# Kernel tuning notes

Measured on AMD Instinct MI355X. Metric: run time of the kernel, lower is better.

Reference implementation:

```python
import jax, jax.numpy as jnp
import numpy as np

# Dimensions
B, S = 4, 1024            # sequences, tokens per sequence (prefill: q_len == kv_len)
NQO, NKV, D = 32, 8, 128  # GQA heads
BS = 16                   # page (block) size
NUM_BLOCKS = 512
BLOCKS_PER_SEQ = S // BS  # 64
SCALE = 1.0 / float(np.sqrt(D))


def setup_inputs() -> dict:
    key = jax.random.key(0)
    k1, k2, k3 = jax.random.split(key, 3)
    query = jax.random.normal(k1, (B * S, NQO * D), dtype=jnp.float32)
    key_t = jax.random.normal(k2, (B * S, NKV * D), dtype=jnp.float32)
    value = jax.random.normal(k3, (B * S, NKV * D), dtype=jnp.float32)

    # Paged layout: each sequence owns BLOCKS_PER_SEQ distinct blocks (shuffled).
    rng = np.random.default_rng(0)
    perm = rng.permutation(NUM_BLOCKS)[: B * BLOCKS_PER_SEQ]
    block_tables = perm.reshape(B, BLOCKS_PER_SEQ).astype(np.int32)
    tok = np.arange(S)
    # flat slot index for token t of sequence b: block_id * BS + offset
    slots = block_tables[:, tok // BS] * BS + (tok % BS)  # [B, S]
    new_cache_slots = jnp.asarray(slots.reshape(-1), dtype=jnp.int32)

    key_cache = jnp.zeros((NUM_BLOCKS, BS, NKV, D), dtype=jnp.float32)
    value_cache = jnp.zeros((NUM_BLOCKS, BS, NKV, D), dtype=jnp.float32)
    return {
        "query": query,
        "key": key_t,
        "value": value,
        "key_cache": key_cache,
        "value_cache": value_cache,
        "new_cache_slots": new_cache_slots,
        "block_tables": jnp.asarray(block_tables),
    }


def reference(query, key, value, key_cache, value_cache, new_cache_slots, block_tables):
    q = query.reshape(B * S, NQO, D)
    k = key.reshape(B * S, NKV, D)
    v = value.reshape(B * S, NKV, D)

    # Scatter new K/V into paged cache (kv_cache.set_kv_cache)
    kc = key_cache.reshape(NUM_BLOCKS * BS, NKV, D).at[new_cache_slots].set(k)
    vc = value_cache.reshape(NUM_BLOCKS * BS, NKV, D).at[new_cache_slots].set(v)

    # Gather per-sequence contiguous KV via block tables
    slot = (block_tables[:, :, None] * BS + jnp.arange(BS)).reshape(B, S)  # [B,S]
    kseq = kc[slot]  # [B, S, NKV, D]
    vseq = vc[slot]  # [B, S, NKV, D]

    G = NQO // NKV
    qb = q.reshape(B, S, NKV, G, D)
    scores = jnp.einsum("bqhgd,bkhd->bhgqk", qb, kseq) * SCALE

    # causal mask (q_len == kv_len here; general rule: k_pos <= kv_len - q_len + q_pos)
    qpos = jnp.arange(S)[:, None]
    kpos = jnp.arange(S)[None, :]
    scores = jnp.where(qpos >= kpos, scores, -jnp.inf)

    probs = jax.nn.softmax(scores, axis=-1)
    out = jnp.einsum("bhgqk,bkhd->bqhgd", probs, vseq)
    return out.reshape(B * S, NQO * D)
```

## Files before the change

### kernel.cpp

```cpp
#include <hip/hip_runtime.h>

typedef __attribute__((ext_vector_type(8))) short bf16x8;
typedef __attribute__((ext_vector_type(16))) float f32x16;
typedef __attribute__((ext_vector_type(4))) unsigned uint4v;
typedef __attribute__((ext_vector_type(2))) unsigned uint2v;

#define MFMA32(a, b, c) __builtin_amdgcn_mfma_f32_32x32x16_bf16((a), (b), (c), 0, 0, 0)

__device__ __forceinline__ unsigned pk2(float lo, float hi) {
  unsigned r;
  asm("v_cvt_pk_bf16_f32 %0, %1, %2" : "=v"(r) : "v"(lo), "v"(hi));
  return r;
}

__device__ __forceinline__ float fexp2(float x) {
  float y; asm("v_exp_f32 %0, %1" : "=v"(y) : "v"(x)); return y;
}

__device__ __forceinline__ f32x16 zero16() {
  f32x16 z;
#pragma unroll
  for (int i = 0; i < 16; ++i) z[i] = 0.0f;
  return z;
}

constexpr int S_ = 1024, D = 128;
constexpr int QSTR = 32 * 128;
constexpr int KSTR = 8 * 128;
constexpr float QSCL = 0.12751741f;

__global__ __launch_bounds__(512, 2) void fa_kernel(
    const float* __restrict__ Qg, const float* __restrict__ Kg,
    const float* __restrict__ Vg, float* __restrict__ Og) {
  const int bid  = blockIdx.x;
  const int hkv  = bid & 7;
  const int b    = (bid >> 3) & 3;
  const int qt64 = 15 - (bid >> 5);
  const int h4   = hkv << 2;

  const int tid  = threadIdx.x;
  const int wid  = tid >> 6;
  const int lane = tid & 63;
  const int r    = lane & 31;
  const int hi   = lane >> 5;

  const int g     = wid & 3;
  const int strip = wid >> 2;
  const int h     = h4 + g;
  const int wq0   = (qt64 << 6) + (strip << 5);
  const int qrow  = wq0 + r;

  __shared__ __align__(16) unsigned char Kl0[64 * 256];
  __shared__ __align__(16) unsigned char Vl0[128 * 128];
  __shared__ __align__(16) unsigned char Kl1[64 * 256];
  __shared__ __align__(16) unsigned char Vl1[128 * 128];

  bf16x8 qf[8];
  {
    const float* qp = Qg + (size_t)(b * S_ + qrow) * QSTR + h * D;
#pragma unroll
    for (int c = 0; c < 8; ++c) {
      const float4* p4 = (const float4*)(qp + 16 * c + 8 * hi);
      float4 x = p4[0], y = p4[1];
      uint4v w = (uint4v){pk2(x.x * QSCL, x.y * QSCL), pk2(x.z * QSCL, x.w * QSCL),
                          pk2(y.x * QSCL, y.y * QSCL), pk2(y.z * QSCL, y.w * QSCL)};
      qf[c] = __builtin_bit_cast(bf16x8, w);
    }
  }

  const int kvrow = tid >> 3;
  const int dbase = (tid & 7) << 4;
  const float* kbase = Kg + (size_t)(b * S_) * KSTR + hkv * D;
  const int vd   = tid & 127;
  const int vkvb = (tid >> 7) << 4;
  const float* vbase = Vg + (size_t)(b * S_) * KSTR + hkv * D;

  float4 kreg[4];
  float  vreg[16];

  auto ISSUE = [&](int kv0) {
    const float4* kp = (const float4*)(kbase + (size_t)(kv0 + kvrow) * KSTR + dbase);
#pragma unroll
    for (int j = 0; j < 4; ++j) kreg[j] = kp[j];
    const float* vp = vbase + (size_t)(kv0 + vkvb) * KSTR + vd;
#pragma unroll
    for (int kk = 0; kk < 16; ++kk) vreg[kk] = vp[kk * KSTR];
  };

  auto WRITE = [&](unsigned char* Kl, unsigned char* Vl) {
#pragma unroll
    for (int ss = 0; ss < 2; ++ss) {
      float4 x = kreg[2 * ss], y = kreg[2 * ss + 1];
      uint4v w = (uint4v){pk2(x.x, x.y), pk2(x.z, x.w), pk2(y.x, y.y), pk2(y.z, y.w)};
      const int slot = (dbase >> 3) + ss;
      *(uint4v*)(Kl + kvrow * 256 + ((slot ^ (kvrow & 7)) << 4)) = w;
    }
#pragma unroll
    for (int ss = 0; ss < 2; ++ss) {
      uint4v w = (uint4v){pk2(vreg[8 * ss + 0], vreg[8 * ss + 1]),
                          pk2(vreg[8 * ss + 2], vreg[8 * ss + 3]),
                          pk2(vreg[8 * ss + 4], vreg[8 * ss + 5]),
                          pk2(vreg[8 * ss + 6], vreg[8 * ss + 7])};
      const int slot = (vkvb >> 3) + ss;
      *(uint4v*)(Vl + vd * 128 + ((slot ^ (vd & 7)) << 4)) = w;
    }
  };

  f32x16 o0 = zero16(), o1 = zero16(), o2 = zero16(), o3 = zero16();
  float m = -1e30f, lsum = 0.0f;

  auto COMPUTE = [&](const unsigned char* Kl, const unsigned char* Vl, int kv0) {
    f32x16 s0 = zero16(), s1 = zero16();
    __builtin_amdgcn_s_setprio(1);
#pragma unroll
    for (int c = 0; c < 8; ++c) {
      const int so = (((2 * c + hi) ^ (r & 7)) << 4);
      bf16x8 k0 = *(const bf16x8*)(Kl + r * 256 + so);
      bf16x8 k1 = *(const bf16x8*)(Kl + (32 + r) * 256 + so);
      s0 = MFMA32(k0, qf[c], s0);
      s1 = MFMA32(k1, qf[c], s1);
    }
    __builtin_amdgcn_s_setprio(0);

    if (kv0 + 63 > wq0) {
#pragma unroll
      for (int rr = 0; rr < 16; ++rr) {
        const int R = (rr & 3) + ((rr >> 2) << 3) + (hi << 2);
        if (kv0 + R > qrow)      s0[rr] = -1e30f;
        if (kv0 + 32 + R > qrow) s1[rr] = -1e30f;
      }
    }

    float mt = fmaxf(s0[0], s1[0]);
#pragma unroll
    for (int rr = 1; rr < 16; ++rr) mt = fmaxf(mt, fmaxf(s0[rr], s1[rr]));
    mt = fmaxf(mt, __shfl_xor(mt, 32));

    if (__any(mt > m + 6.0f)) {
      const float mn = fmaxf(m, mt);
      const float sc = fexp2(m - mn);
      m = mn;
      lsum *= sc;
#pragma unroll
      for (int rr = 0; rr < 16; ++rr) {
        const float srow = __shfl(sc, (rr & 3) + ((rr >> 2) << 3) + (hi << 2));
        o0[rr] *= srow; o1[rr] *= srow; o2[rr] *= srow; o3[rr] *= srow;
      }
    }

    float ps = 0.0f;
    bf16x8 A0, A1, A2, A3;
    {
      float p[16];
#pragma unroll
      for (int rr = 0; rr < 16; ++rr) { p[rr] = fexp2(s0[rr] - m); ps += p[rr]; }
      unsigned d0 = pk2(p[0], p[1]),   d1 = pk2(p[2], p[3]);
      unsigned d2 = pk2(p[4], p[5]),   d3 = pk2(p[6], p[7]);
      unsigned d4 = pk2(p[8], p[9]),   d5 = pk2(p[10], p[11]);
      unsigned d6 = pk2(p[12], p[13]), d7 = pk2(p[14], p[15]);
      uint2v w02 = __builtin_amdgcn_permlane32_swap(d0, d2, false, false);
      uint2v w13 = __builtin_amdgcn_permlane32_swap(d1, d3, false, false);
      uint2v w46 = __builtin_amdgcn_permlane32_swap(d4, d6, false, false);
      uint2v w57 = __builtin_amdgcn_permlane32_swap(d5, d7, false, false);
      A0 = __builtin_bit_cast(bf16x8, (uint4v){w02[0], w13[0], w02[1], w13[1]});
      A1 = __builtin_bit_cast(bf16x8, (uint4v){w46[0], w57[0], w46[1], w57[1]});
    }
    {
      float p[16];
#pragma unroll
      for (int rr = 0; rr < 16; ++rr) { p[rr] = fexp2(s1[rr] - m); ps += p[rr]; }
      unsigned d0 = pk2(p[0], p[1]),   d1 = pk2(p[2], p[3]);
      unsigned d2 = pk2(p[4], p[5]),   d3 = pk2(p[6], p[7]);
      unsigned d4 = pk2(p[8], p[9]),   d5 = pk2(p[10], p[11]);
      unsigned d6 = pk2(p[12], p[13]), d7 = pk2(p[14], p[15]);
      uint2v w02 = __builtin_amdgcn_permlane32_swap(d0, d2, false, false);
      uint2v w13 = __builtin_amdgcn_permlane32_swap(d1, d3, false, false);
      uint2v w46 = __builtin_amdgcn_permlane32_swap(d4, d6, false, false);
      uint2v w57 = __builtin_amdgcn_permlane32_swap(d5, d7, false, false);
      A2 = __builtin_bit_cast(bf16x8, (uint4v){w02[0], w13[0], w02[1], w13[1]});
      A3 = __builtin_bit_cast(bf16x8, (uint4v){w46[0], w57[0], w46[1], w57[1]});
    }
    lsum += ps;

    __builtin_amdgcn_s_setprio(1);
#pragma unroll
    for (int t = 0; t < 4; ++t) {
      const bf16x8 pf = (t == 0) ? A0 : (t == 1) ? A1 : (t == 2) ? A2 : A3;
      const int so = (((2 * t + hi) ^ (r & 7)) << 4);
      bf16x8 v0 = *(const bf16x8*)(Vl + r * 128 + so);
      bf16x8 v1 = *(const bf16x8*)(Vl + (32 + r) * 128 + so);
      bf16x8 v2 = *(const bf16x8*)(Vl + (64 + r) * 128 + so);
      bf16x8 v3 = *(const bf16x8*)(Vl + (96 + r) * 128 + so);
      o0 = MFMA32(pf, v0, o0);
      o1 = MFMA32(pf, v1, o1);
      o2 = MFMA32(pf, v2, o2);
      o3 = MFMA32(pf, v3, o3);
    }
    __builtin_amdgcn_s_setprio(0);
  };

  const int nt = qt64 + 1;

  ISSUE(0);
  WRITE(Kl0, Vl0);
  if (nt > 1) ISSUE(64);

  unsigned char *Kc = Kl0, *Vc = Vl0, *Kn = Kl1, *Vn = Vl1;
  for (int t = 0; t < nt; ++t) {
    __syncthreads();
    COMPUTE(Kc, Vc, t << 6);
    if (t + 1 < nt) {
      WRITE(Kn, Vn);
      if (t + 2 < nt) ISSUE((t + 2) << 6);
      unsigned char* tp;
      tp = Kc; Kc = Kn; Kn = tp;
      tp = Vc; Vc = Vn; Vn = tp;
    }
  }

  float lt = lsum + __shfl_xor(lsum, 32);
#pragma unroll
  for (int rr = 0; rr < 16; ++rr) {
    const int R = (rr & 3) + ((rr >> 2) << 3) + (hi << 2);
    const float li = __shfl(lt, R);
    const float inv = 1.0f / li;
    float* op = Og + (size_t)(b * S_ + wq0 + R) * QSTR + h * D + r;
    op[0]  = o0[rr] * inv;
    op[32] = o1[rr] * inv;
    op[64] = o2[rr] * inv;
    op[96] = o3[rr] * inv;
  }
}

extern "C" void kernel_launch(void* const* d_in, const int* in_sizes, int n_in,
                              void* d_out, int out_size, void* d_ws, size_t ws_size,
                              hipStream_t stream) {
  const float* Q = (const float*)d_in[0];
  const float* K = (const float*)d_in[1];
  const float* V = (const float*)d_in[2];
  float* O = (float*)d_out;
  fa_kernel<<<dim3(512), dim3(512), 0, stream>>>(Q, K, V, O);
}
```

Baseline: 63.59 us.

## Switch to 16x16x32 MFMA with 16 waves per block and staggered load/compute

Replaces the 32x32x16 MFMA tiling with 16x16x32 MFMAs, so each wave handles 16 query rows and the block grows to 1024 threads (16 waves), halving per-thread K/V staging and accumulator registers. The P-to-A-operand relayout now uses shuffles instead of permlane32 swaps. Alternate strips order the global-to-LDS write before or after compute to spread memory and MFMA activity. This raises occupancy and parallelism but adds shuffle overhead, and each K/V LDS tile is now read by twice as many waves.

```diff
diff --git a/kernel.cpp b/kernel.cpp
--- a/kernel.cpp
+++ b/kernel.cpp
@@ -1,11 +1,10 @@
 #include <hip/hip_runtime.h>
 
 typedef __attribute__((ext_vector_type(8))) short bf16x8;
-typedef __attribute__((ext_vector_type(16))) float f32x16;
+typedef __attribute__((ext_vector_type(4))) float f32x4;
 typedef __attribute__((ext_vector_type(4))) unsigned uint4v;
-typedef __attribute__((ext_vector_type(2))) unsigned uint2v;
-
-#define MFMA32(a, b, c) __builtin_amdgcn_mfma_f32_32x32x16_bf16((a), (b), (c), 0, 0, 0)
+
+#define MFMA16(a, b, c) __builtin_amdgcn_mfma_f32_16x16x32_bf16((a), (b), (c), 0, 0, 0)
 
 __device__ __forceinline__ unsigned pk2(float lo, float hi) {
   unsigned r;
@@ -17,11 +16,8 @@
   float y; asm("v_exp_f32 %0, %1" : "=v"(y) : "v"(x)); return y;
 }
 
-__device__ __forceinline__ f32x16 zero16() {
-  f32x16 z;
-#pragma unroll
-  for (int i = 0; i < 16; ++i) z[i] = 0.0f;
-  return z;
+__device__ __forceinline__ f32x4 zero4() {
+  return (f32x4){0.0f, 0.0f, 0.0f, 0.0f};
 }
 
 constexpr int S_ = 1024, D = 128;
@@ -29,38 +25,37 @@
 constexpr int KSTR = 8 * 128;
 constexpr float QSCL = 0.12751741f;
 
-__global__ __launch_bounds__(512, 2) void fa_kernel(
+__global__ __launch_bounds__(1024, 4) void fa_kernel(
     const float* __restrict__ Qg, const float* __restrict__ Kg,
     const float* __restrict__ Vg, float* __restrict__ Og) {
   const int bid  = blockIdx.x;
   const int hkv  = bid & 7;
   const int b    = (bid >> 3) & 3;
   const int qt64 = 15 - (bid >> 5);
-  const int h4   = hkv << 2;
 
   const int tid  = threadIdx.x;
   const int wid  = tid >> 6;
   const int lane = tid & 63;
-  const int r    = lane & 31;
-  const int hi   = lane >> 5;
+  const int q16  = lane & 15;
+  const int lg   = lane >> 4;
 
   const int g     = wid & 3;
   const int strip = wid >> 2;
-  const int h     = h4 + g;
-  const int wq0   = (qt64 << 6) + (strip << 5);
-  const int qrow  = wq0 + r;
+  const int h     = (hkv << 2) + g;
+  const int wq0   = (qt64 << 6) + (strip << 4);
+  const int qrow  = wq0 + q16;
 
   __shared__ __align__(16) unsigned char Kl0[64 * 256];
   __shared__ __align__(16) unsigned char Vl0[128 * 128];
   __shared__ __align__(16) unsigned char Kl1[64 * 256];
   __shared__ __align__(16) unsigned char Vl1[128 * 128];
 
-  bf16x8 qf[8];
+  bf16x8 qf[4];
   {
     const float* qp = Qg + (size_t)(b * S_ + qrow) * QSTR + h * D;
 #pragma unroll
-    for (int c = 0; c < 8; ++c) {
-      const float4* p4 = (const float4*)(qp + 16 * c + 8 * hi);
+    for (int c = 0; c < 4; ++c) {
+      const float4* p4 = (const float4*)(qp + 32 * c + 8 * lg);
       float4 x = p4[0], y = p4[1];
       uint4v w = (uint4v){pk2(x.x * QSCL, x.y * QSCL), pk2(x.z * QSCL, x.w * QSCL),
                           pk2(y.x * QSCL, y.y * QSCL), pk2(y.z * QSCL, y.w * QSCL)};
@@ -68,72 +63,73 @@
     }
   }
 
-  const int kvrow = tid >> 3;
-  const int dbase = (tid & 7) << 4;
+  const int kvrow = tid >> 4;
+  const int dbase = (tid & 15) << 3;
   const float* kbase = Kg + (size_t)(b * S_) * KSTR + hkv * D;
   const int vd   = tid & 127;
-  const int vkvb = (tid >> 7) << 4;
+  const int vkvb = (tid >> 7) << 3;
   const float* vbase = Vg + (size_t)(b * S_) * KSTR + hkv * D;
 
-  float4 kreg[4];
-  float  vreg[16];
+  float4 kreg[2];
+  float  vreg[8];
 
   auto ISSUE = [&](int kv0) {
     const float4* kp = (const float4*)(kbase + (size_t)(kv0 + kvrow) * KSTR + dbase);
-#pragma unroll
-    for (int j = 0; j < 4; ++j) kreg[j] = kp[j];
+    kreg[0] = kp[0];
+    kreg[1] = kp[1];
     const float* vp = vbase + (size_t)(kv0 + vkvb) * KSTR + vd;
 #pragma unroll
-    for (int kk = 0; kk < 16; ++kk) vreg[kk] = vp[kk * KSTR];
+    for (int kk = 0; kk < 8; ++kk) vreg[kk] = vp[kk * KSTR];
   };
 
   auto WRITE = [&](unsigned char* Kl, unsigned char* Vl) {
-#pragma unroll
-    for (int ss = 0; ss < 2; ++ss) {
-      float4 x = kreg[2 * ss], y = kreg[2 * ss + 1];
-      uint4v w = (uint4v){pk2(x.x, x.y), pk2(x.z, x.w), pk2(y.x, y.y), pk2(y.z, y.w)};
-      const int slot = (dbase >> 3) + ss;
-      *(uint4v*)(Kl + kvrow * 256 + ((slot ^ (kvrow & 7)) << 4)) = w;
-    }
-#pragma unroll
-    for (int ss = 0; ss < 2; ++ss) {
-      uint4v w = (uint4v){pk2(vreg[8 * ss + 0], vreg[8 * ss + 1]),
-                          pk2(vreg[8 * ss + 2], vreg[8 * ss + 3]),
-                          pk2(vreg[8 * ss + 4], vreg[8 * ss + 5]),
-                          pk2(vreg[8 * ss + 6], vreg[8 * ss + 7])};
-      const int slot = (vkvb >> 3) + ss;
-      *(uint4v*)(Vl + vd * 128 + ((slot ^ (vd & 7)) << 4)) = w;
-    }
+    uint4v wk = (uint4v){pk2(kreg[0].x, kreg[0].y), pk2(kreg[0].z, kreg[0].w),
+                         pk2(kreg[1].x, kreg[1].y), pk2(kreg[1].z, kreg[1].w)};
+    *(uint4v*)(Kl + kvrow * 256 + (((tid & 15) ^ (kvrow & 7)) << 4)) = wk;
+    uint4v wv = (uint4v){pk2(vreg[0], vreg[1]), pk2(vreg[2], vreg[3]),
+                         pk2(vreg[4], vreg[5]), pk2(vreg[6], vreg[7])};
+    *(uint4v*)(Vl + vd * 128 + (((tid >> 7) ^ (vd & 7)) << 4)) = wv;
   };
 
-  f32x16 o0 = zero16(), o1 = zero16(), o2 = zero16(), o3 = zero16();
+  f32x4 o0 = zero4(), o1 = zero4(), o2 = zero4(), o3 = zero4();
+  f32x4 o4 = zero4(), o5 = zero4(), o6 = zero4(), o7 = zero4();
   float m = -1e30f, lsum = 0.0f;
 
   auto COMPUTE = [&](const unsigned char* Kl, const unsigned char* Vl, int kv0) {
-    f32x16 s0 = zero16(), s1 = zero16();
+    f32x4 s0 = zero4(), s1 = zero4(), s2 = zero4(), s3 = zero4();
     __builtin_amdgcn_s_setprio(1);
 #pragma unroll
-    for (int c = 0; c < 8; ++c) {
-      const int so = (((2 * c + hi) ^ (r & 7)) << 4);
-      bf16x8 k0 = *(const bf16x8*)(Kl + r * 256 + so);
-      bf16x8 k1 = *(const bf16x8*)(Kl + (32 + r) * 256 + so);
-      s0 = MFMA32(k0, qf[c], s0);
-      s1 = MFMA32(k1, qf[c], s1);
+    for (int c = 0; c < 4; ++c) {
+      const int so = ((4 * c + lg) ^ (q16 & 7)) << 4;
+      const unsigned char* Kb = Kl + q16 * 256 + so;
+      bf16x8 k0 = *(const bf16x8*)(Kb);
+      bf16x8 k1 = *(const bf16x8*)(Kb + 16 * 256);
+      bf16x8 k2 = *(const bf16x8*)(Kb + 32 * 256);
+      bf16x8 k3 = *(const bf16x8*)(Kb + 48 * 256);
+      s0 = MFMA16(k0, qf[c], s0);
+      s1 = MFMA16(k1, qf[c], s1);
+      s2 = MFMA16(k2, qf[c], s2);
+      s3 = MFMA16(k3, qf[c], s3);
     }
     __builtin_amdgcn_s_setprio(0);
 
     if (kv0 + 63 > wq0) {
+      const int kvb_ = kv0 + 4 * lg;
 #pragma unroll
-      for (int rr = 0; rr < 16; ++rr) {
-        const int R = (rr & 3) + ((rr >> 2) << 3) + (hi << 2);
-        if (kv0 + R > qrow)      s0[rr] = -1e30f;
-        if (kv0 + 32 + R > qrow) s1[rr] = -1e30f;
+      for (int reg = 0; reg < 4; ++reg) {
+        if (kvb_ + reg > qrow)      s0[reg] = -1e30f;
+        if (kvb_ + 16 + reg > qrow) s1[reg] = -1e30f;
+        if (kvb_ + 32 + reg > qrow) s2[reg] = -1e30f;
+        if (kvb_ + 48 + reg > qrow) s3[reg] = -1e30f;
       }
     }
 
-    float mt = fmaxf(s0[0], s1[0]);
-#pragma unroll
-    for (int rr = 1; rr < 16; ++rr) mt = fmaxf(mt, fmaxf(s0[rr], s1[rr]));
+    float x0 = fmaxf(fmaxf(s0[0], s1[0]), fmaxf(s2[0], s3[0]));
+    float x1 = fmaxf(fmaxf(s0[1], s1[1]), fmaxf(s2[1], s3[1]));
+    float x2 = fmaxf(fmaxf(s0[2], s1[2]), fmaxf(s2[2], s3[2]));
+    float x3 = fmaxf(fmaxf(s0[3], s1[3]), fmaxf(s2[3], s3[3]));
+    float mt = fmaxf(fmaxf(x0, x1), fmaxf(x2, x3));
+    mt = fmaxf(mt, __shfl_xor(mt, 16));
     mt = fmaxf(mt, __shfl_xor(mt, 32));
 
     if (__any(mt > m + 6.0f)) {
@@ -141,60 +137,110 @@
       const float sc = fexp2(m - mn);
       m = mn;
       lsum *= sc;
-#pragma unroll
-      for (int rr = 0; rr < 16; ++rr) {
-        const float srow = __shfl(sc, (rr & 3) + ((rr >> 2) << 3) + (hi << 2));
-        o0[rr] *= srow; o1[rr] *= srow; o2[rr] *= srow; o3[rr] *= srow;
-      }
-    }
-
-    float ps = 0.0f;
-    bf16x8 A0, A1, A2, A3;
-    {
-      float p[16];
-#pragma unroll
-      for (int rr = 0; rr < 16; ++rr) { p[rr] = fexp2(s0[rr] - m); ps += p[rr]; }
-      unsigned d0 = pk2(p[0], p[1]),   d1 = pk2(p[2], p[3]);
-      unsigned d2 = pk2(p[4], p[5]),   d3 = pk2(p[6], p[7]);
-      unsigned d4 = pk2(p[8], p[9]),   d5 = pk2(p[10], p[11]);
-      unsigned d6 = pk2(p[12], p[13]), d7 = pk2(p[14], p[15]);
-      uint2v w02 = __builtin_amdgcn_permlane32_swap(d0, d2, false, false);
-      uint2v w13 = __builtin_amdgcn_permlane32_swap(d1, d3, false, false);
-      uint2v w46 = __builtin_amdgcn_permlane32_swap(d4, d6, false, false);
-      uint2v w57 = __builtin_amdgcn_permlane32_swap(d5, d7, false, false);
-      A0 = __builtin_bit_cast(bf16x8, (uint4v){w02[0], w13[0], w02[1], w13[1]});
-      A1 = __builtin_bit_cast(bf16x8, (uint4v){w46[0], w57[0], w46[1], w57[1]});
-    }
-    {
-      float p[16];
-#pragma unroll
-      for (int rr = 0; rr < 16; ++rr) { p[rr] = fexp2(s1[rr] - m); ps += p[rr]; }
-      unsigned d0 = pk2(p[0], p[1]),   d1 = pk2(p[2], p[3]);
-      unsigned d2 = pk2(p[4], p[5]),   d3 = pk2(p[6], p[7]);
-      unsigned d4 = pk2(p[8], p[9]),   d5 = pk2(p[10], p[11]);
-      unsigned d6 = pk2(p[12], p[13]), d7 = pk2(p[14], p[15]);
-      uint2v w02 = __builtin_amdgcn_permlane32_swap(d0, d2, false, false);
-      uint2v w13 = __builtin_amdgcn_permlane32_swap(d1, d3, false, false);
-      uint2v w46 = __builtin_amdgcn_permlane32_swap(d4, d6, false, false);
-      uint2v w57 = __builtin_amdgcn_permlane32_swap(d5, d7, false, false);
-      A2 = __builtin_bit_cast(bf16x8, (uint4v){w02[0], w13[0], w02[1], w13[1]});
-      A3 = __builtin_bit_cast(bf16x8, (uint4v){w46[0], w57[0], w46[1], w57[1]});
-    }
-    lsum += ps;
+      const float c0 = __shfl(sc, 4 * lg + 0);
+      const float c1 = __shfl(sc, 4 * lg + 1);
+      const float c2 = __shfl(sc, 4 * lg + 2);
+      const float c3 = __shfl(sc, 4 * lg + 3);
+      o0[0] *= c0; o0[1] *= c1; o0[2] *= c2; o0[3] *= c3;
+      o1[0] *= c0; o1[1] *= c1; o1[2] *= c2; o1[3] *= c3;
+      o2[0] *= c0; o2[1] *= c1; o2[2] *= c2; o2[3] *= c3;
+      o3[0] *= c0; o3[1] *= c1; o3[2] *= c2; o3[3] *= c3;
+      o4[0] *= c0; o4[1] *= c1; o4[2] *= c2; o4[3] *= c3;
+      o5[0] *= c0; o5[1] *= c1; o5[2] *= c2; o5[3] *= c3;
+      o6[0] *= c0; o6[1] *= c1; o6[2] *= c2; o6[3] *= c3;
+      o7[0] *= c0; o7[1] *= c1; o7[2] *= c2; o7[3] *= c3;
+    }
+
+    unsigned wA0, wB0, wA1, wB1, wA2, wB2, wA3, wB3;
+    {
+      float p0 = fexp2(s0[0] - m), p1 = fexp2(s0[1] - m);
+      float p2 = fexp2(s0[2] - m), p3 = fexp2(s0[3] - m);
+      lsum += (p0 + p1) + (p2 + p3);
+      wA0 = pk2(p0, p1); wB0 = pk2(p2, p3);
+    }
+    {
+      float p0 = fexp2(s1[0] - m), p1 = fexp2(s1[1] - m);
+      float p2 = fexp2(s1[2] - m), p3 = fexp2(s1[3] - m);
+      lsum += (p0 + p1) + (p2 + p3);
+      wA1 = pk2(p0, p1); wB1 = pk2(p2, p3);
+    }
+    {
+      float p0 = fexp2(s2[0] - m), p1 = fexp2(s2[1] - m);
+      float p2 = fexp2(s2[2] - m), p3 = fexp2(s2[3] - m);
+      lsum += (p0 + p1) + (p2 + p3);
+      wA2 = pk2(p0, p1); wB2 = pk2(p2, p3);
+    }
+    {
+      float p0 = fexp2(s3[0] - m), p1 = fexp2(s3[1] - m);
+      float p2 = fexp2(s3[2] - m), p3 = fexp2(s3[3] - m);
+      lsum += (p0 + p1) + (p2 + p3);
+      wA3 = pk2(p0, p1); wB3 = pk2(p2, p3);
+    }
+
+    const int src0 = q16 + ((lg & 1) << 5);
+    const int src1 = src0 + 16;
+    const bool uh = (lane >= 32);
+    bf16x8 A0, A1;
+    {
+      unsigned e0 = __shfl(wA0, src0), f0 = __shfl(wA1, src0);
+      unsigned e1 = __shfl(wB0, src0), f1 = __shfl(wB1, src0);
+      unsigned e2 = __shfl(wA0, src1), f2 = __shfl(wA1, src1);
+      unsigned e3 = __shfl(wB0, src1), f3 = __shfl(wB1, src1);
+      uint4v a = (uint4v){uh ? f0 : e0, uh ? f1 : e1, uh ? f2 : e2, uh ? f3 : e3};
+      A0 = __builtin_bit_cast(bf16x8, a);
+    }
+    {
+      unsigned e0 = __shfl(wA2, src0), f0 = __shfl(wA3, src0);
+      unsigned e1 = __shfl(wB2, src0), f1 = __shfl(wB3, src0);
+      unsigned e2 = __shfl(wA2, src1), f2 = __shfl(wA3, src1);
+      unsigned e3 = __shfl(wB2, src1), f3 = __shfl(wB3, src1);
+      uint4v a = (uint4v){uh ? f0 : e0, uh ? f1 : e1, uh ? f2 : e2, uh ? f3 : e3};
+      A1 = __builtin_bit_cast(bf16x8, a);
+    }
 
     __builtin_amdgcn_s_setprio(1);
-#pragma unroll
-    for (int t = 0; t < 4; ++t) {
-      const bf16x8 pf = (t == 0) ? A0 : (t == 1) ? A1 : (t == 2) ? A2 : A3;
-      const int so = (((2 * t + hi) ^ (r & 7)) << 4);
-      bf16x8 v0 = *(const bf16x8*)(Vl + r * 128 + so);
-      bf16x8 v1 = *(const bf16x8*)(Vl + (32 + r) * 128 + so);
-      bf16x8 v2 = *(const bf16x8*)(Vl + (64 + r) * 128 + so);
-      bf16x8 v3 = *(const bf16x8*)(Vl + (96 + r) * 128 + so);
-      o0 = MFMA32(pf, v0, o0);
-      o1 = MFMA32(pf, v1, o1);
-      o2 = MFMA32(pf, v2, o2);
-      o3 = MFMA32(pf, v3, o3);
+    const int vso0 = (lg ^ (q16 & 7)) << 4;
+    const int vso1 = ((4 + lg) ^ (q16 & 7)) << 4;
+    const unsigned char* Vb = Vl + q16 * 128;
+    {
+      bf16x8 v0 = *(const bf16x8*)(Vb + 0 * 2048 + vso0);
+      bf16x8 v1 = *(const bf16x8*)(Vb + 0 * 2048 + vso1);
+      o0 = MFMA16(A0, v0, o0); o0 = MFMA16(A1, v1, o0);
+    }
+    {
+      bf16x8 v0 = *(const bf16x8*)(Vb + 1 * 2048 + vso0);
+      bf16x8 v1 = *(const bf16x8*)(Vb + 1 * 2048 + vso1);
+      o1 = MFMA16(A0, v0, o1); o1 = MFMA16(A1, v1, o1);
+    }
+    {
+      bf16x8 v0 = *(const bf16x8*)(Vb + 2 * 2048 + vso0);
+      bf16x8 v1 = *(const bf16x8*)(Vb + 2 * 2048 + vso1);
+      o2 = MFMA16(A0, v0, o2); o2 = MFMA16(A1, v1, o2);
+    }
+    {
+      bf16x8 v0 = *(const bf16x8*)(Vb + 3 * 2048 + vso0);
+      bf16x8 v1 = *(const bf16x8*)(Vb + 3 * 2048 + vso1);
+      o3 = MFMA16(A0, v0, o3); o3 = MFMA16(A1, v1, o3);
+    }
+    {
+      bf16x8 v0 = *(const bf16x8*)(Vb + 4 * 2048 + vso0);
+      bf16x8 v1 = *(const bf16x8*)(Vb + 4 * 2048 + vso1);
+      o4 = MFMA16(A0, v0, o4); o4 = MFMA16(A1, v1, o4);
+    }
+    {
+      bf16x8 v0 = *(const bf16x8*)(Vb + 5 * 2048 + vso0);
+      bf16x8 v1 = *(const bf16x8*)(Vb + 5 * 2048 + vso1);
+      o5 = MFMA16(A0, v0, o5); o5 = MFMA16(A1, v1, o5);
+    }
+    {
+      bf16x8 v0 = *(const bf16x8*)(Vb + 6 * 2048 + vso0);
+      bf16x8 v1 = *(const bf16x8*)(Vb + 6 * 2048 + vso1);
+      o6 = MFMA16(A0, v0, o6); o6 = MFMA16(A1, v1, o6);
+    }
+    {
+      bf16x8 v0 = *(const bf16x8*)(Vb + 7 * 2048 + vso0);
+      bf16x8 v1 = *(const bf16x8*)(Vb + 7 * 2048 + vso1);
+      o7 = MFMA16(A0, v0, o7); o7 = MFMA16(A1, v1, o7);
     }
     __builtin_amdgcn_s_setprio(0);
   };
@@ -208,28 +254,49 @@
   unsigned char *Kc = Kl0, *Vc = Vl0, *Kn = Kl1, *Vn = Vl1;
   for (int t = 0; t < nt; ++t) {
     __syncthreads();
-    COMPUTE(Kc, Vc, t << 6);
+    if ((strip & 1) == 0) {
+      COMPUTE(Kc, Vc, t << 6);
+      if (t + 1 < nt) {
+        WRITE(Kn, Vn);
+        if (t + 2 < nt) ISSUE((t + 2) << 6);
+      }
+    } else {
+      if (t + 1 < nt) {
+        WRITE(Kn, Vn);
+        if (t + 2 < nt) ISSUE((t + 2) << 6);
+      }
+      COMPUTE(Kc, Vc, t << 6);
+    }
     if (t + 1 < nt) {
-      WRITE(Kn, Vn);
-      if (t + 2 < nt) ISSUE((t + 2) << 6);
       unsigned char* tp;
       tp = Kc; Kc = Kn; Kn = tp;
       tp = Vc; Vc = Vn; Vn = tp;
     }
   }
 
-  float lt = lsum + __shfl_xor(lsum, 32);
-#pragma unroll
-  for (int rr = 0; rr < 16; ++rr) {
-    const int R = (rr & 3) + ((rr >> 2) << 3) + (hi << 2);
-    const float li = __shfl(lt, R);
-    const float inv = 1.0f / li;
-    float* op = Og + (size_t)(b * S_ + wq0 + R) * QSTR + h * D + r;
-    op[0]  = o0[rr] * inv;
-    op[32] = o1[rr] * inv;
-    op[64] = o2[rr] * inv;
-    op[96] = o3[rr] * inv;
-  }
+  float lt = lsum + __shfl_xor(lsum, 16);
+  lt += __shfl_xor(lt, 32);
+  const float i0 = 1.0f / __shfl(lt, 4 * lg + 0);
+  const float i1 = 1.0f / __shfl(lt, 4 * lg + 1);
+  const float i2 = 1.0f / __shfl(lt, 4 * lg + 2);
+  const float i3 = 1.0f / __shfl(lt, 4 * lg + 3);
+  float* op = Og + (size_t)(b * S_ + wq0 + 4 * lg) * QSTR + h * D + q16;
+  op[0 * QSTR +   0] = o0[0] * i0; op[1 * QSTR +   0] = o0[1] * i1;
+  op[2 * QSTR +   0] = o0[2] * i2; op[3 * QSTR +   0] = o0[3] * i3;
+  op[0 * QSTR +  16] = o1[0] * i0; op[1 * QSTR +  16] = o1[1] * i1;
+  op[2 * QSTR +  16] = o1[2] * i2; op[3 * QSTR +  16] = o1[3] * i3;
+  op[0 * QSTR +  32] = o2[0] * i0; op[1 * QSTR +  32] = o2[1] * i1;
+  op[2 * QSTR +  32] = o2[2] * i2; op[3 * QSTR +  32] = o2[3] * i3;
+  op[0 * QSTR +  48] = o3[0] * i0; op[1 * QSTR +  48] = o3[1] * i1;
+  op[2 * QSTR +  48] = o3[2] * i2; op[3 * QSTR +  48] = o3[3] * i3;
+  op[0 * QSTR +  64] = o4[0] * i0; op[1 * QSTR +  64] = o4[1] * i1;
+  op[2 * QSTR +  64] = o4[2] * i2; op[3 * QSTR +  64] = o4[3] * i3;
+  op[0 * QSTR +  80] = o5[0] * i0; op[1 * QSTR +  80] = o5[1] * i1;
+  op[2 * QSTR +  80] = o5[2] * i2; op[3 * QSTR +  80] = o5[3] * i3;
+  op[0 * QSTR +  96] = o6[0] * i0; op[1 * QSTR +  96] = o6[1] * i1;
+  op[2 * QSTR +  96] = o6[2] * i2; op[3 * QSTR +  96] = o6[3] * i3;
+  op[0 * QSTR + 112] = o7[0] * i0; op[1 * QSTR + 112] = o7[1] * i1;
+  op[2 * QSTR + 112] = o7[2] * i2; op[3 * QSTR + 112] = o7[3] * i3;
 }
 
 extern "C" void kernel_launch(void* const* d_in, const int* in_sizes, int n_in,
@@ -239,5 +306,5 @@
   const float* K = (const float*)d_in[1];
   const float* V = (const float*)d_in[2];
   float* O = (float*)d_out;
-  fa_kernel<<<dim3(512), dim3(512), 0, stream>>>(Q, K, V, O);
-}
+  fa_kernel<<<dim3(512), dim3(1024), 0, stream>>>(Q, K, V, O);
+}
```

Measured after the change: 68.88 us. 8.3% more time.
